# Optimization experiments

Hardware: AMD Instinct MI355X
Metric: run time of the kernel (lower is better)

Reference implementation:

```python
import jax, jax.numpy as jnp
import numpy as np

D_MODEL = 1024
N_HEADS = 16
HEAD_DIM = D_MODEL // N_HEADS

def setup_inputs() -> dict:
    key = jax.random.key(0)
    ks = jax.random.split(key, 12)
    s = 0.02
    return {
        "x": jax.random.normal(ks[0], (2, 2048, D_MODEL), dtype=jnp.float32),
        "ln1_w": jnp.ones((D_MODEL,), jnp.float32),
        "ln1_b": jnp.zeros((D_MODEL,), jnp.float32),
        "ln2_w": jnp.ones((D_MODEL,), jnp.float32),
        "ln2_b": jnp.zeros((D_MODEL,), jnp.float32),
        "w_attn": jax.random.normal(ks[1], (D_MODEL, 3 * D_MODEL), jnp.float32) * s,
        "b_attn": jnp.zeros((3 * D_MODEL,), jnp.float32),
        "w_proj": jax.random.normal(ks[2], (D_MODEL, D_MODEL), jnp.float32) * s,
        "b_proj": jnp.zeros((D_MODEL,), jnp.float32),
        "w_fc": jax.random.normal(ks[3], (D_MODEL, 4 * D_MODEL), jnp.float32) * s,
        "b_fc": jnp.zeros((4 * D_MODEL,), jnp.float32),
        "w_fc2": jax.random.normal(ks[4], (4 * D_MODEL, D_MODEL), jnp.float32) * s,
        "b_fc2": jnp.zeros((D_MODEL,), jnp.float32),
    }

def _layernorm(x, w, b, eps=1e-5):
    mu = jnp.mean(x, axis=-1, keepdims=True)
    var = jnp.var(x, axis=-1, keepdims=True)
    return (x - mu) * jax.lax.rsqrt(var + eps) * w + b

def reference(x, ln1_w, ln1_b, ln2_w, ln2_b, w_attn, b_attn, w_proj, b_proj,
              w_fc, b_fc, w_fc2, b_fc2):
    B, T, C = x.shape
    # --- attention branch ---
    h = _layernorm(x, ln1_w, ln1_b)
    qkv = h @ w_attn + b_attn                      # [B,T,3C]
    q, k, v = jnp.split(qkv, 3, axis=-1)
    q = q.reshape(B, T, N_HEADS, HEAD_DIM).transpose(0, 2, 1, 3)  # [B,H,T,d]
    k = k.reshape(B, T, N_HEADS, HEAD_DIM).transpose(0, 2, 1, 3)
    v = v.reshape(B, T, N_HEADS, HEAD_DIM).transpose(0, 2, 1, 3)
    att = jnp.einsum('bhqd,bhkd->bhqk', q, k) / jnp.sqrt(jnp.float32(HEAD_DIM))
    causal = jnp.tril(jnp.ones((T, T), dtype=bool))
    att = jnp.where(causal, att, jnp.float32(-jnp.inf))
    att = jax.nn.softmax(att, axis=-1)
    y = jnp.einsum('bhqk,bhkd->bhqd', att, v)      # [B,H,T,d]
    y = y.transpose(0, 2, 1, 3).reshape(B, T, C)
    x = x + (y @ w_proj + b_proj)
    # --- MLP branch ---
    h = _layernorm(x, ln2_w, ln2_b)
    h = jax.nn.gelu(h @ w_fc + b_fc, approximate=False)
    x = x + (h @ w_fc2 + b_fc2)
    return x
```

## Files before the change

kernel.cpp:

```cpp
#include <hip/hip_runtime.h>
#include <cstdint>
#include <cstddef>


#define D_MODEL 1024
#define TSEQ    2048
#define BATCH   2
#define NHEADS  16
#define NTOK    (BATCH*TSEQ)

typedef __attribute__((ext_vector_type(8))) short bf16x8;
typedef __attribute__((ext_vector_type(4))) float f32x4;
typedef unsigned short ushort_t;

#define AS3(p) ((__attribute__((address_space(3))) unsigned int*)(p))
#define AS1(p) ((const __attribute__((address_space(1))) unsigned int*)(p))

__device__ __forceinline__ unsigned short f2bf(float f){
  union { float f; unsigned u; } v; v.f = f;
  unsigned r = v.u + 0x7fffu + ((v.u >> 16) & 1u);
  return (unsigned short)(r >> 16);
}
__device__ __forceinline__ unsigned pk2bf(float a, float b){
  union { float f; unsigned u; } x, y; x.f = a; y.f = b;
  return __builtin_amdgcn_perm(y.u + 0x8000u, x.u + 0x8000u, 0x07060302u);
}

__global__ __launch_bounds__(256) void wtrans_all(
    const float* __restrict__ w0, ushort_t* __restrict__ o0,
    const float* __restrict__ w1, ushort_t* __restrict__ o1,
    const float* __restrict__ w2, ushort_t* __restrict__ o2,
    const float* __restrict__ w3, ushort_t* __restrict__ o3){
  __shared__ float tile[32][33];
  int bid = blockIdx.x;
  const float* in; ushort_t* out; int K, N, t;
  if (bid < 3072)      { in=w0; out=o0; K=1024; N=3072; t=bid; }
  else if (bid < 4096) { in=w1; out=o1; K=1024; N=1024; t=bid-3072; }
  else if (bid < 8192) { in=w2; out=o2; K=1024; N=4096; t=bid-4096; }
  else                 { in=w3; out=o3; K=4096; N=1024; t=bid-8192; }
  int tx_n = N >> 5;
  int n0 = (t % tx_n)*32, k0 = (t / tx_n)*32;
  int tx = threadIdx.x & 31, ty = threadIdx.x >> 5;
  #pragma unroll
  for (int i=0;i<32;i+=8)
    tile[ty+i][tx] = in[(size_t)(k0+ty+i)*N + n0+tx];
  __syncthreads();
  #pragma unroll
  for (int i=0;i<32;i+=8)
    out[(size_t)(n0+ty+i)*K + k0+tx] = f2bf(tile[tx][ty+i]);
}

__global__ __launch_bounds__(256) void ln_kernel(const float* __restrict__ x,
                                                 const float* __restrict__ w,
                                                 const float* __restrict__ b,
                                                 ushort_t* __restrict__ out){
  int row = blockIdx.x;
  int tid = threadIdx.x;
  const float* xr = x + (size_t)row*D_MODEL;
  float4 v = ((const float4*)xr)[tid];
  float s  = v.x+v.y+v.z+v.w;
  float s2 = v.x*v.x+v.y*v.y+v.z*v.z+v.w*v.w;
  #pragma unroll
  for (int off=1; off<64; off<<=1){ s += __shfl_xor(s,off); s2 += __shfl_xor(s2,off); }
  __shared__ float ss[4], ss2[4];
  int wave = tid>>6, lane = tid&63;
  if (lane==0){ ss[wave]=s; ss2[wave]=s2; }
  __syncthreads();
  s  = ss[0]+ss[1]+ss[2]+ss[3];
  s2 = ss2[0]+ss2[1]+ss2[2]+ss2[3];
  float mu  = s * (1.0f/D_MODEL);
  float var = s2 * (1.0f/D_MODEL) - mu*mu;
  float rstd = rsqrtf(var + 1e-5f);
  float4 wv = ((const float4*)w)[tid];
  float4 bv = ((const float4*)b)[tid];
  uint2 pk;
  pk.x = pk2bf((v.x-mu)*rstd*wv.x + bv.x, (v.y-mu)*rstd*wv.y + bv.y);
  pk.y = pk2bf((v.z-mu)*rstd*wv.z + bv.z, (v.w-mu)*rstd*wv.w + bv.w);
  *(uint2*)(out + (size_t)row*D_MODEL + tid*4) = pk;
}

template<int MODE, int BN>
__global__ __launch_bounds__(256, 4) void gemm_bt(const ushort_t* __restrict__ A,
                                                  const ushort_t* __restrict__ BT,
                                                  const float* __restrict__ bias,
                                                  const float* __restrict__ res,
                                                  void* __restrict__ out,
                                                  int M, int N, int K){
  constexpr int NI = BN/32;
  constexpr int BG = BN/32;
  __shared__ __align__(16) ushort_t As[128*64];
  __shared__ __align__(16) ushort_t Bs[BN*64];
  const int m0 = blockIdx.x*128, n0 = blockIdx.y*BN;
  const int tid = threadIdx.x;
  const int wave = tid >> 6, lane = tid & 63;
  const int wm = (wave >> 1)*64, wn = (wave & 1)*(BN/2);
  const int quad = lane >> 4, l16 = lane & 15;

  f32x4 acc[4][NI] = {};

  for (int k0 = 0; k0 < K; k0 += 64) {
    #pragma unroll
    for (int c = 0; c < 4; ++c) {
      int q   = (c*4 + wave)*64 + lane;
      int row = q >> 3, pos = q & 7;
      int lc  = pos ^ (row & 7);
      __builtin_amdgcn_global_load_lds(AS1(A + (size_t)(m0+row)*K + k0 + lc*8),
                                       AS3(&As[(c*4+wave)*512]), 16, 0, 0);
    }
    #pragma unroll
    for (int c = 0; c < BG; ++c) {
      int q   = (c*4 + wave)*64 + lane;
      int row = q >> 3, pos = q & 7;
      int lc  = pos ^ (row & 7);
      __builtin_amdgcn_global_load_lds(AS1(BT + (size_t)(n0+row)*K + k0 + lc*8),
                                       AS3(&Bs[(c*4+wave)*512]), 16, 0, 0);
    }
    __syncthreads();
    #pragma unroll
    for (int kk = 0; kk < 64; kk += 32) {
      bf16x8 af[4], bfr[NI];
      #pragma unroll
      for (int i = 0; i < 4; ++i){
        int row = wm + i*16 + l16;
        int pos = ((kk>>3) + quad) ^ (row & 7);
        af[i] = *(const bf16x8*)(&As[row*64 + pos*8]);
      }
      #pragma unroll
      for (int i = 0; i < NI; ++i){
        int row = wn + i*16 + l16;
        int pos = ((kk>>3) + quad) ^ (row & 7);
        bfr[i] = *(const bf16x8*)(&Bs[row*64 + pos*8]);
      }
      #pragma unroll
      for (int mi = 0; mi < 4; ++mi)
        #pragma unroll
        for (int ni = 0; ni < NI; ++ni)
          acc[mi][ni] = __builtin_amdgcn_mfma_f32_16x16x32_bf16(bfr[ni], af[mi], acc[mi][ni], 0,0,0);
    }
    __syncthreads();
  }

  #pragma unroll
  for (int ni = 0; ni < NI; ++ni){
    int nb = n0 + wn + ni*16 + quad*4;
    float4 b4 = *(const float4*)(bias + nb);
    #pragma unroll
    for (int mi = 0; mi < 4; ++mi){
      int row = m0 + wm + mi*16 + l16;
      float v0 = acc[mi][ni][0] + b4.x;
      float v1 = acc[mi][ni][1] + b4.y;
      float v2 = acc[mi][ni][2] + b4.z;
      float v3 = acc[mi][ni][3] + b4.w;
      if constexpr (MODE == 1){
        const float4 r4 = *(const float4*)(res + (size_t)row*N + nb);
        float4 o4 = make_float4(v0+r4.x, v1+r4.y, v2+r4.z, v3+r4.w);
        *(float4*)((float*)out + (size_t)row*N + nb) = o4;
      } else if constexpr (MODE == 2){
        float g0 = 0.5f*v0*(1.0f + erff(v0*0.70710678118654752f));
        float g1 = 0.5f*v1*(1.0f + erff(v1*0.70710678118654752f));
        float g2 = 0.5f*v2*(1.0f + erff(v2*0.70710678118654752f));
        float g3 = 0.5f*v3*(1.0f + erff(v3*0.70710678118654752f));
        uint2 pk; pk.x = pk2bf(g0,g1); pk.y = pk2bf(g2,g3);
        *(uint2*)((ushort_t*)out + (size_t)row*N + nb) = pk;
      } else {
        uint2 pk; pk.x = pk2bf(v0,v1); pk.y = pk2bf(v2,v3);
        *(uint2*)((ushort_t*)out + (size_t)row*N + nb) = pk;
      }
    }
  }
}

#define LDSS 72
__global__ __launch_bounds__(256) void vtrans(const ushort_t* __restrict__ qkv,
                                              ushort_t* __restrict__ vt){
  __shared__ __align__(16) ushort_t tile[64*LDSS];
  const int bh = blockIdx.x;
  const int b = bh >> 4, h = bh & 15;
  const int t0 = blockIdx.y*64;
  const int tid = threadIdx.x;
  #pragma unroll
  for (int it = 0; it < 2; ++it){
    int idx = it*256 + tid;
    int i = idx >> 3, c = (idx & 7) << 3;
    uint4 vv = *(const uint4*)(qkv + (size_t)(b*TSEQ + t0 + i)*3072 + 2048 + h*64 + c);
    *(uint4*)(&tile[i*LDSS + c]) = vv;
  }
  __syncthreads();
  #pragma unroll
  for (int it = 0; it < 2; ++it){
    int idx = it*256 + tid;
    int j = idx >> 3, ii = (idx & 7) << 3;
    union { unsigned short us[8]; uint4 u4; } pk;
    #pragma unroll
    for (int e = 0; e < 8; ++e) pk.us[e] = tile[(ii+e)*LDSS + j];
    *(uint4*)(vt + (size_t)(bh*64 + j)*TSEQ + t0 + ii) = pk.u4;
  }
}

#define PSTR 72
__global__ __launch_bounds__(256) void attn_kernel(const ushort_t* __restrict__ qkv,
                                                   const ushort_t* __restrict__ vt,
                                                   ushort_t* __restrict__ y){
  __shared__ __align__(16) ushort_t Ks[2][64*64];
  __shared__ __align__(16) ushort_t Vs[2][64*64];
  __shared__ __align__(16) ushort_t Plds[4][16*PSTR];
  const int bh = blockIdx.x;
  const int b = bh >> 4, h = bh & 15;
  const int qt = (TSEQ/64 - 1) - blockIdx.y;
  const int q0 = qt * 64;
  const int wave = threadIdx.x >> 6, lane = threadIdx.x & 63;
  const int quad = lane >> 4, l16 = lane & 15;
  const int qrow = q0 + wave*16 + l16;

  const ushort_t* qbase = qkv + (size_t)(b*TSEQ)*3072 + h*64;
  const ushort_t* kbase = qbase + 1024;
  const ushort_t* vbase = vt + (size_t)(bh*64)*TSEQ;
  ushort_t* P = Plds[wave];

  auto stage = [&](int buf, int j0){
    #pragma unroll
    for (int c = 0; c < 2; ++c){
      int q = (wave*2 + c)*64 + lane;
      int row = q >> 3, pos = q & 7;
      int lc = pos ^ (row & 7);
      __builtin_amdgcn_global_load_lds(AS1(kbase + (size_t)(j0+row)*3072 + lc*8),
                                       AS3(&Ks[buf][(wave*2+c)*512]), 16, 0, 0);
      __builtin_amdgcn_global_load_lds(AS1(vbase + (size_t)row*TSEQ + j0 + lc*8),
                                       AS3(&Vs[buf][(wave*2+c)*512]), 16, 0, 0);
    }
  };

  bf16x8 qf[2];
  #pragma unroll
  for (int kk = 0; kk < 2; ++kk)
    qf[kk] = *(const bf16x8*)(qbase + (size_t)qrow*3072 + kk*32 + quad*8);

  float m_i = -3e38f, l_i = 0.f;
  f32x4 o[4] = {};
  const float cs = 0.18033688011112042f;

  const int ntiles = qt + 1;
  stage(0, 0);
  for (int it = 0; it < ntiles; ++it) {
    const int cur = it & 1;
    const int j0 = it * 64;
    __syncthreads();
    if (it + 1 < ntiles) stage(cur ^ 1, j0 + 64);
    f32x4 s[4] = {};
    #pragma unroll
    for (int kk = 0; kk < 2; ++kk){
      #pragma unroll
      for (int nj = 0; nj < 4; ++nj){
        int row = nj*16 + l16;
        int pos = (kk*4 + quad) ^ (row & 7);
        bf16x8 kf = *(const bf16x8*)(&Ks[cur][row*64 + pos*8]);
        s[nj] = __builtin_amdgcn_mfma_f32_16x16x32_bf16(kf, qf[kk], s[nj], 0,0,0);
      }
    }
    if (it == ntiles-1) {
      #pragma unroll
      for (int nj = 0; nj < 4; ++nj)
        #pragma unroll
        for (int r = 0; r < 4; ++r){
          int jc = j0 + nj*16 + quad*4 + r;
          if (jc > qrow) s[nj][r] = -3e38f;
        }
    }
    float mloc = s[0][0];
    #pragma unroll
    for (int nj = 0; nj < 4; ++nj)
      #pragma unroll
      for (int r = 0; r < 4; ++r) mloc = fmaxf(mloc, s[nj][r]);
    mloc = fmaxf(mloc, __shfl_xor(mloc, 16));
    mloc = fmaxf(mloc, __shfl_xor(mloc, 32));
    float mn = fmaxf(m_i, mloc);
    float alpha = __builtin_amdgcn_exp2f((m_i - mn)*cs);
    m_i = mn;
    float rs = 0.f;
    #pragma unroll
    for (int nj = 0; nj < 4; ++nj){
      float p0 = __builtin_amdgcn_exp2f((s[nj][0]-mn)*cs);
      float p1 = __builtin_amdgcn_exp2f((s[nj][1]-mn)*cs);
      float p2 = __builtin_amdgcn_exp2f((s[nj][2]-mn)*cs);
      float p3 = __builtin_amdgcn_exp2f((s[nj][3]-mn)*cs);
      rs += (p0+p1)+(p2+p3);
      uint2 pk; pk.x = pk2bf(p0,p1); pk.y = pk2bf(p2,p3);
      *(uint2*)(&P[l16*PSTR + nj*16 + quad*4]) = pk;
    }
    rs += __shfl_xor(rs, 16);
    rs += __shfl_xor(rs, 32);
    l_i = l_i*alpha + rs;
    #pragma unroll
    for (int dj = 0; dj < 4; ++dj)
      #pragma unroll
      for (int r = 0; r < 4; ++r) o[dj][r] *= alpha;
    bf16x8 pf[2];
    #pragma unroll
    for (int kk = 0; kk < 2; ++kk)
      pf[kk] = *(const bf16x8*)(&P[l16*PSTR + kk*32 + quad*8]);
    #pragma unroll
    for (int kk = 0; kk < 2; ++kk){
      #pragma unroll
      for (int dj = 0; dj < 4; ++dj){
        int row = dj*16 + l16;
        int pos = (kk*4 + quad) ^ (row & 7);
        bf16x8 vf = *(const bf16x8*)(&Vs[cur][row*64 + pos*8]);
        o[dj] = __builtin_amdgcn_mfma_f32_16x16x32_bf16(vf, pf[kk], o[dj], 0,0,0);
      }
    }
  }
  float inv = 1.0f / l_i;
  ushort_t* yr = y + (size_t)(b*TSEQ + qrow)*D_MODEL + h*64;
  #pragma unroll
  for (int dj = 0; dj < 4; ++dj){
    uint2 pk;
    pk.x = pk2bf(o[dj][0]*inv, o[dj][1]*inv);
    pk.y = pk2bf(o[dj][2]*inv, o[dj][3]*inv);
    *(uint2*)(yr + dj*16 + quad*4) = pk;
  }
}

extern "C" void kernel_launch(void* const* d_in, const int* in_sizes, int n_in,
                              void* d_out, int out_size, void* d_ws, size_t ws_size,
                              hipStream_t stream)
{
  (void)in_sizes; (void)n_in; (void)out_size; (void)ws_size;
  const float* x      = (const float*)d_in[0];
  const float* ln1_w  = (const float*)d_in[1];
  const float* ln1_b  = (const float*)d_in[2];
  const float* ln2_w  = (const float*)d_in[3];
  const float* ln2_b  = (const float*)d_in[4];
  const float* w_attn = (const float*)d_in[5];
  const float* b_attn = (const float*)d_in[6];
  const float* w_proj = (const float*)d_in[7];
  const float* b_proj = (const float*)d_in[8];
  const float* w_fc   = (const float*)d_in[9];
  const float* b_fc   = (const float*)d_in[10];
  const float* w_fc2  = (const float*)d_in[11];
  const float* b_fc2  = (const float*)d_in[12];
  float* out = (float*)d_out;

  char* p = (char*)d_ws;
  auto alloc = [&](size_t n){ char* r = p; p += (n + 255) & ~(size_t)255; return (void*)r; };
  ushort_t* wAT  = (ushort_t*)alloc((size_t)3072*1024*2);
  ushort_t* wPT  = (ushort_t*)alloc((size_t)1024*1024*2);
  ushort_t* wFT  = (ushort_t*)alloc((size_t)4096*1024*2);
  ushort_t* wF2T = (ushort_t*)alloc((size_t)1024*4096*2);
  ushort_t* hbuf = (ushort_t*)alloc((size_t)NTOK*D_MODEL*2);
  ushort_t* qkv  = (ushort_t*)alloc((size_t)NTOK*4096*2);
  ushort_t* vt   = (ushort_t*)alloc((size_t)32*64*TSEQ*2);
  ushort_t* ybuf = (ushort_t*)alloc((size_t)NTOK*D_MODEL*2);
  float*    x1   = (float*)   alloc((size_t)NTOK*D_MODEL*4);
  ushort_t* hh   = qkv;

  wtrans_all<<<12288, 256, 0, stream>>>(w_attn, wAT, w_proj, wPT, w_fc, wFT, w_fc2, wF2T);

  ln_kernel<<<NTOK, 256, 0, stream>>>(x, ln1_w, ln1_b, hbuf);
  gemm_bt<0,128><<<dim3(NTOK/128, 3072/128), 256, 0, stream>>>(hbuf, wAT, b_attn, nullptr, qkv, NTOK, 3072, 1024);
  vtrans<<<dim3(32, TSEQ/64), 256, 0, stream>>>(qkv, vt);
  attn_kernel<<<dim3(32, TSEQ/64), 256, 0, stream>>>(qkv, vt, ybuf);
  gemm_bt<1,64><<<dim3(NTOK/128, 1024/64), 256, 0, stream>>>(ybuf, wPT, b_proj, x, x1, NTOK, 1024, 1024);
  ln_kernel<<<NTOK, 256, 0, stream>>>(x1, ln2_w, ln2_b, hbuf);
  gemm_bt<2,128><<<dim3(NTOK/128, 4096/128), 256, 0, stream>>>(hbuf, wFT, b_fc, nullptr, hh, NTOK, 4096, 1024);
  gemm_bt<1,64><<<dim3(NTOK/128, 1024/64), 256, 0, stream>>>(hh, wF2T, b_fc2, x1, out, NTOK, 1024, 4096);
}
```

Baseline: 347.2 us.

## Stage GEMM epilogues through LDS and process two query groups per attention block

The GEMM epilogue now writes results into shared memory (reusing the operand tile space) and then emits row-contiguous 16-byte global stores, with residual reads coalesced in MODE 1. The attention kernel now handles 128 query rows per block as two 64-row groups sharing each staged K/V tile, which halves K/V global loads per query and halves the grid. The costs are more registers for the doubled accumulators, extra barriers in the epilogue, fewer blocks in the attention launch, and one idle group on the final tile.

```diff
diff --git a/kernel.cpp b/kernel.cpp
--- a/kernel.cpp
+++ b/kernel.cpp
@@ -88,8 +88,12 @@
                                                   int M, int N, int K){
   constexpr int NI = BN/32;
   constexpr int BG = BN/32;
-  __shared__ __align__(16) ushort_t As[128*64];
-  __shared__ __align__(16) ushort_t Bs[BN*64];
+  constexpr int KBYTES = 128*64*2 + BN*64*2;
+  constexpr int CBYTES = (MODE==1) ? 64*66*4 : 128*132*2;
+  constexpr int SBYTES = (KBYTES > CBYTES) ? KBYTES : CBYTES;
+  __shared__ __align__(16) char smem[SBYTES];
+  ushort_t* As = (ushort_t*)smem;
+  ushort_t* Bs = As + 128*64;
   const int m0 = blockIdx.x*128, n0 = blockIdx.y*BN;
   const int tid = threadIdx.x;
   const int wave = tid >> 6, lane = tid & 63;
@@ -140,32 +144,71 @@
     __syncthreads();
   }
 
-  #pragma unroll
-  for (int ni = 0; ni < NI; ++ni){
-    int nb = n0 + wn + ni*16 + quad*4;
-    float4 b4 = *(const float4*)(bias + nb);
-    #pragma unroll
-    for (int mi = 0; mi < 4; ++mi){
-      int row = m0 + wm + mi*16 + l16;
-      float v0 = acc[mi][ni][0] + b4.x;
-      float v1 = acc[mi][ni][1] + b4.y;
-      float v2 = acc[mi][ni][2] + b4.z;
-      float v3 = acc[mi][ni][3] + b4.w;
-      if constexpr (MODE == 1){
-        const float4 r4 = *(const float4*)(res + (size_t)row*N + nb);
-        float4 o4 = make_float4(v0+r4.x, v1+r4.y, v2+r4.z, v3+r4.w);
-        *(float4*)((float*)out + (size_t)row*N + nb) = o4;
-      } else if constexpr (MODE == 2){
-        float g0 = 0.5f*v0*(1.0f + erff(v0*0.70710678118654752f));
-        float g1 = 0.5f*v1*(1.0f + erff(v1*0.70710678118654752f));
-        float g2 = 0.5f*v2*(1.0f + erff(v2*0.70710678118654752f));
-        float g3 = 0.5f*v3*(1.0f + erff(v3*0.70710678118654752f));
-        uint2 pk; pk.x = pk2bf(g0,g1); pk.y = pk2bf(g2,g3);
-        *(uint2*)((ushort_t*)out + (size_t)row*N + nb) = pk;
-      } else {
+  if constexpr (MODE == 1) {
+    float* Cf = (float*)smem;
+    #pragma unroll
+    for (int ph = 0; ph < 2; ++ph){
+      if (ph) __syncthreads();
+      if (wm == ph*64) {
+        #pragma unroll
+        for (int ni = 0; ni < NI; ++ni){
+          int cb = wn + ni*16 + quad*4;
+          float4 b4 = *(const float4*)(bias + n0 + cb);
+          #pragma unroll
+          for (int mi = 0; mi < 4; ++mi){
+            int lm = mi*16 + l16;
+            float2 v01 = make_float2(acc[mi][ni][0] + b4.x, acc[mi][ni][1] + b4.y);
+            float2 v23 = make_float2(acc[mi][ni][2] + b4.z, acc[mi][ni][3] + b4.w);
+            *(float2*)(&Cf[lm*66 + cb])     = v01;
+            *(float2*)(&Cf[lm*66 + cb + 2]) = v23;
+          }
+        }
+      }
+      __syncthreads();
+      int lr = tid >> 2, qq = tid & 3;
+      size_t grow = (size_t)(m0 + ph*64 + lr)*N + n0;
+      #pragma unroll
+      for (int jj = 0; jj < 4; ++jj){
+        int cc = (jj*4 + qq)*4;
+        float2 a  = *(float2*)(&Cf[lr*66 + cc]);
+        float2 c2 = *(float2*)(&Cf[lr*66 + cc + 2]);
+        float4 r4 = *(const float4*)(res + grow + cc);
+        float4 o4 = make_float4(a.x + r4.x, a.y + r4.y, c2.x + r4.z, c2.y + r4.w);
+        *(float4*)((float*)out + grow + cc) = o4;
+      }
+    }
+  } else {
+    ushort_t* Cs = (ushort_t*)smem;
+    #pragma unroll
+    for (int ni = 0; ni < NI; ++ni){
+      int cb = wn + ni*16 + quad*4;
+      float4 b4 = *(const float4*)(bias + n0 + cb);
+      #pragma unroll
+      for (int mi = 0; mi < 4; ++mi){
+        int m = wm + mi*16 + l16;
+        float v0 = acc[mi][ni][0] + b4.x;
+        float v1 = acc[mi][ni][1] + b4.y;
+        float v2 = acc[mi][ni][2] + b4.z;
+        float v3 = acc[mi][ni][3] + b4.w;
+        if constexpr (MODE == 2){
+          v0 = 0.5f*v0*(1.0f + erff(v0*0.70710678118654752f));
+          v1 = 0.5f*v1*(1.0f + erff(v1*0.70710678118654752f));
+          v2 = 0.5f*v2*(1.0f + erff(v2*0.70710678118654752f));
+          v3 = 0.5f*v3*(1.0f + erff(v3*0.70710678118654752f));
+        }
         uint2 pk; pk.x = pk2bf(v0,v1); pk.y = pk2bf(v2,v3);
-        *(uint2*)((ushort_t*)out + (size_t)row*N + nb) = pk;
-      }
+        *(uint2*)(&Cs[m*132 + cb]) = pk;
+      }
+    }
+    __syncthreads();
+    int r = tid >> 1, hh2 = tid & 1;
+    size_t grow = (size_t)(m0 + r)*N + n0 + hh2*64;
+    #pragma unroll
+    for (int jj = 0; jj < 8; ++jj){
+      uint2 a  = *(uint2*)(&Cs[r*132 + hh2*64 + jj*8]);
+      uint2 b2 = *(uint2*)(&Cs[r*132 + hh2*64 + jj*8 + 4]);
+      uint4 o4 = make_uint4(a.x, a.y, b2.x, b2.y);
+      *(uint4*)((ushort_t*)out + grow + jj*8) = o4;
     }
   }
 }
@@ -206,11 +249,10 @@
   __shared__ __align__(16) ushort_t Plds[4][16*PSTR];
   const int bh = blockIdx.x;
   const int b = bh >> 4, h = bh & 15;
-  const int qt = (TSEQ/64 - 1) - blockIdx.y;
-  const int q0 = qt * 64;
+  const int qt = (TSEQ/128 - 1) - blockIdx.y;
+  const int q0 = qt * 128;
   const int wave = threadIdx.x >> 6, lane = threadIdx.x & 63;
   const int quad = lane >> 4, l16 = lane & 15;
-  const int qrow = q0 + wave*16 + l16;
 
   const ushort_t* qbase = qkv + (size_t)(b*TSEQ)*3072 + h*64;
   const ushort_t* kbase = qbase + 1024;
@@ -230,93 +272,105 @@
     }
   };
 
-  bf16x8 qf[2];
-  #pragma unroll
-  for (int kk = 0; kk < 2; ++kk)
-    qf[kk] = *(const bf16x8*)(qbase + (size_t)qrow*3072 + kk*32 + quad*8);
-
-  float m_i = -3e38f, l_i = 0.f;
-  f32x4 o[4] = {};
+  int qrow[2];
+  bf16x8 qf[2][2];
+  #pragma unroll
+  for (int g = 0; g < 2; ++g){
+    qrow[g] = q0 + g*64 + wave*16 + l16;
+    #pragma unroll
+    for (int kk = 0; kk < 2; ++kk)
+      qf[g][kk] = *(const bf16x8*)(qbase + (size_t)qrow[g]*3072 + kk*32 + quad*8);
+  }
+
+  float m_i[2] = {-3e38f, -3e38f}, l_i[2] = {0.f, 0.f};
+  f32x4 o[2][4] = {};
   const float cs = 0.18033688011112042f;
 
-  const int ntiles = qt + 1;
+  const int ntiles = 2*qt + 2;
   stage(0, 0);
   for (int it = 0; it < ntiles; ++it) {
     const int cur = it & 1;
     const int j0 = it * 64;
     __syncthreads();
     if (it + 1 < ntiles) stage(cur ^ 1, j0 + 64);
-    f32x4 s[4] = {};
-    #pragma unroll
-    for (int kk = 0; kk < 2; ++kk){
+    #pragma unroll
+    for (int g = 0; g < 2; ++g){
+      if (g == 0 && it == ntiles-1) continue;
+      f32x4 s[4] = {};
+      #pragma unroll
+      for (int kk = 0; kk < 2; ++kk){
+        #pragma unroll
+        for (int nj = 0; nj < 4; ++nj){
+          int row = nj*16 + l16;
+          int pos = (kk*4 + quad) ^ (row & 7);
+          bf16x8 kf = *(const bf16x8*)(&Ks[cur][row*64 + pos*8]);
+          s[nj] = __builtin_amdgcn_mfma_f32_16x16x32_bf16(kf, qf[g][kk], s[nj], 0,0,0);
+        }
+      }
+      if (it >= ntiles-2) {
+        #pragma unroll
+        for (int nj = 0; nj < 4; ++nj)
+          #pragma unroll
+          for (int r = 0; r < 4; ++r){
+            int jc = j0 + nj*16 + quad*4 + r;
+            if (jc > qrow[g]) s[nj][r] = -3e38f;
+          }
+      }
+      float mloc = s[0][0];
+      #pragma unroll
+      for (int nj = 0; nj < 4; ++nj)
+        #pragma unroll
+        for (int r = 0; r < 4; ++r) mloc = fmaxf(mloc, s[nj][r]);
+      mloc = fmaxf(mloc, __shfl_xor(mloc, 16));
+      mloc = fmaxf(mloc, __shfl_xor(mloc, 32));
+      float mn = fmaxf(m_i[g], mloc);
+      float alpha = __builtin_amdgcn_exp2f((m_i[g] - mn)*cs);
+      m_i[g] = mn;
+      float rs = 0.f;
       #pragma unroll
       for (int nj = 0; nj < 4; ++nj){
-        int row = nj*16 + l16;
-        int pos = (kk*4 + quad) ^ (row & 7);
-        bf16x8 kf = *(const bf16x8*)(&Ks[cur][row*64 + pos*8]);
-        s[nj] = __builtin_amdgcn_mfma_f32_16x16x32_bf16(kf, qf[kk], s[nj], 0,0,0);
-      }
-    }
-    if (it == ntiles-1) {
-      #pragma unroll
-      for (int nj = 0; nj < 4; ++nj)
-        #pragma unroll
-        for (int r = 0; r < 4; ++r){
-          int jc = j0 + nj*16 + quad*4 + r;
-          if (jc > qrow) s[nj][r] = -3e38f;
+        float p0 = __builtin_amdgcn_exp2f((s[nj][0]-mn)*cs);
+        float p1 = __builtin_amdgcn_exp2f((s[nj][1]-mn)*cs);
+        float p2 = __builtin_amdgcn_exp2f((s[nj][2]-mn)*cs);
+        float p3 = __builtin_amdgcn_exp2f((s[nj][3]-mn)*cs);
+        rs += (p0+p1)+(p2+p3);
+        uint2 pk; pk.x = pk2bf(p0,p1); pk.y = pk2bf(p2,p3);
+        *(uint2*)(&P[l16*PSTR + nj*16 + quad*4]) = pk;
+      }
+      rs += __shfl_xor(rs, 16);
+      rs += __shfl_xor(rs, 32);
+      l_i[g] = l_i[g]*alpha + rs;
+      #pragma unroll
+      for (int dj = 0; dj < 4; ++dj)
+        #pragma unroll
+        for (int r = 0; r < 4; ++r) o[g][dj][r] *= alpha;
+      bf16x8 pf[2];
+      #pragma unroll
+      for (int kk = 0; kk < 2; ++kk)
+        pf[kk] = *(const bf16x8*)(&P[l16*PSTR + kk*32 + quad*8]);
+      #pragma unroll
+      for (int kk = 0; kk < 2; ++kk){
+        #pragma unroll
+        for (int dj = 0; dj < 4; ++dj){
+          int row = dj*16 + l16;
+          int pos = (kk*4 + quad) ^ (row & 7);
+          bf16x8 vf = *(const bf16x8*)(&Vs[cur][row*64 + pos*8]);
+          o[g][dj] = __builtin_amdgcn_mfma_f32_16x16x32_bf16(vf, pf[kk], o[g][dj], 0,0,0);
         }
-    }
-    float mloc = s[0][0];
-    #pragma unroll
-    for (int nj = 0; nj < 4; ++nj)
-      #pragma unroll
-      for (int r = 0; r < 4; ++r) mloc = fmaxf(mloc, s[nj][r]);
-    mloc = fmaxf(mloc, __shfl_xor(mloc, 16));
-    mloc = fmaxf(mloc, __shfl_xor(mloc, 32));
-    float mn = fmaxf(m_i, mloc);
-    float alpha = __builtin_amdgcn_exp2f((m_i - mn)*cs);
-    m_i = mn;
-    float rs = 0.f;
-    #pragma unroll
-    for (int nj = 0; nj < 4; ++nj){
-      float p0 = __builtin_amdgcn_exp2f((s[nj][0]-mn)*cs);
-      float p1 = __builtin_amdgcn_exp2f((s[nj][1]-mn)*cs);
-      float p2 = __builtin_amdgcn_exp2f((s[nj][2]-mn)*cs);
-      float p3 = __builtin_amdgcn_exp2f((s[nj][3]-mn)*cs);
-      rs += (p0+p1)+(p2+p3);
-      uint2 pk; pk.x = pk2bf(p0,p1); pk.y = pk2bf(p2,p3);
-      *(uint2*)(&P[l16*PSTR + nj*16 + quad*4]) = pk;
-    }
-    rs += __shfl_xor(rs, 16);
-    rs += __shfl_xor(rs, 32);
-    l_i = l_i*alpha + rs;
-    #pragma unroll
-    for (int dj = 0; dj < 4; ++dj)
-      #pragma unroll
-      for (int r = 0; r < 4; ++r) o[dj][r] *= alpha;
-    bf16x8 pf[2];
-    #pragma unroll
-    for (int kk = 0; kk < 2; ++kk)
-      pf[kk] = *(const bf16x8*)(&P[l16*PSTR + kk*32 + quad*8]);
-    #pragma unroll
-    for (int kk = 0; kk < 2; ++kk){
-      #pragma unroll
-      for (int dj = 0; dj < 4; ++dj){
-        int row = dj*16 + l16;
-        int pos = (kk*4 + quad) ^ (row & 7);
-        bf16x8 vf = *(const bf16x8*)(&Vs[cur][row*64 + pos*8]);
-        o[dj] = __builtin_amdgcn_mfma_f32_16x16x32_bf16(vf, pf[kk], o[dj], 0,0,0);
-      }
-    }
-  }
-  float inv = 1.0f / l_i;
-  ushort_t* yr = y + (size_t)(b*TSEQ + qrow)*D_MODEL + h*64;
-  #pragma unroll
-  for (int dj = 0; dj < 4; ++dj){
-    uint2 pk;
-    pk.x = pk2bf(o[dj][0]*inv, o[dj][1]*inv);
-    pk.y = pk2bf(o[dj][2]*inv, o[dj][3]*inv);
-    *(uint2*)(yr + dj*16 + quad*4) = pk;
+      }
+    }
+  }
+  #pragma unroll
+  for (int g = 0; g < 2; ++g){
+    float inv = 1.0f / l_i[g];
+    ushort_t* yr = y + (size_t)(b*TSEQ + qrow[g])*D_MODEL + h*64;
+    #pragma unroll
+    for (int dj = 0; dj < 4; ++dj){
+      uint2 pk;
+      pk.x = pk2bf(o[g][dj][0]*inv, o[g][dj][1]*inv);
+      pk.y = pk2bf(o[g][dj][2]*inv, o[g][dj][3]*inv);
+      *(uint2*)(yr + dj*16 + quad*4) = pk;
+    }
   }
 }
 
@@ -358,7 +412,7 @@
   ln_kernel<<<NTOK, 256, 0, stream>>>(x, ln1_w, ln1_b, hbuf);
   gemm_bt<0,128><<<dim3(NTOK/128, 3072/128), 256, 0, stream>>>(hbuf, wAT, b_attn, nullptr, qkv, NTOK, 3072, 1024);
   vtrans<<<dim3(32, TSEQ/64), 256, 0, stream>>>(qkv, vt);
-  attn_kernel<<<dim3(32, TSEQ/64), 256, 0, stream>>>(qkv, vt, ybuf);
+  attn_kernel<<<dim3(32, TSEQ/128), 256, 0, stream>>>(qkv, vt, ybuf);
   gemm_bt<1,64><<<dim3(NTOK/128, 1024/64), 256, 0, stream>>>(ybuf, wPT, b_proj, x, x1, NTOK, 1024, 1024);
   ln_kernel<<<NTOK, 256, 0, stream>>>(x1, ln2_w, ln2_b, hbuf);
   gemm_bt<2,128><<<dim3(NTOK/128, 4096/128), 256, 0, stream>>>(hbuf, wFT, b_fc, nullptr, hh, NTOK, 4096, 1024);
```

Measured after the change: 371.5 us. 1.07x slower.
